# Optimization experiments

Hardware: AMD Instinct MI355X
Metric: run time of the kernel (lower is better)

The kernel has to match this reference:

```python
import jax, jax.numpy as jnp
import numpy as np


def setup_inputs() -> dict:
    key = jax.random.key(0)
    k1, k2 = jax.random.split(key)
    B, S, F = 8, 2048, 128
    feature = jax.random.normal(k1, (B, S, F), dtype=jnp.float32)
    noise = jax.random.normal(k2, (B, S, S), dtype=jnp.float32)
    return {"feature": feature, "noise": noise}


def reference(feature, noise):
    # stability: inverse variance over feat dim (torch.var is unbiased -> ddof=1)
    var = jnp.var(feature, axis=2, ddof=1, keepdims=True)          # [B, S, 1]
    stability = 1.0 / (var + 1e-6)
    stability = stability / jnp.max(stability)                      # global max normalize
    # scale per-row noise and softmax over keys (last dim)
    scaled = noise * stability                                      # [B, S, S]
    path = jax.nn.softmax(scaled, axis=-1)                          # [B, S, S]
    # weighted sum of frames
    return jnp.einsum('bij,bjf->bif', path, feature)                # [B, S, F]
```

## Files before the change

### kernel.cpp

```cpp
#include <hip/hip_runtime.h>
#include <hip/hip_bf16.h>

#define BATCH 8
#define SEQ   2048
#define FEATD 128
#define IBLK  32
#define JT    64
#define EPAD  72
#define FPAD  72

typedef __attribute__((ext_vector_type(8))) short short8;
typedef __attribute__((ext_vector_type(4))) float f32x4;

__device__ __forceinline__ unsigned short f2bf(float f) {
  unsigned int u = __float_as_uint(f);
  u += 0x7fffu + ((u >> 16) & 1u);
  return (unsigned short)(u >> 16);
}

__global__ __launch_bounds__(256)
void prep_kernel(const float* __restrict__ feature,
                 float* __restrict__ stab,
                 unsigned int* __restrict__ gmax,
                 unsigned short* __restrict__ featT) {
  __shared__ float tile[32][132];
  __shared__ float wmax[4];
  int bid = blockIdx.x;
  int b   = bid >> 6;
  int j0  = (bid & 63) * 32;
  int t   = threadIdx.x;
  int r   = t >> 3;
  int seg = t & 7;

  const float* rp = feature + ((size_t)(b * SEQ + j0 + r)) * FEATD + seg * 16;
  float s = 0.0f, ss = 0.0f;
  #pragma unroll
  for (int k = 0; k < 4; k++) {
    float4 v = ((const float4*)rp)[k];
    tile[r][seg * 16 + k * 4 + 0] = v.x;
    tile[r][seg * 16 + k * 4 + 1] = v.y;
    tile[r][seg * 16 + k * 4 + 2] = v.z;
    tile[r][seg * 16 + k * 4 + 3] = v.w;
    s  += v.x + v.y + v.z + v.w;
    ss += v.x * v.x + v.y * v.y + v.z * v.z + v.w * v.w;
  }
  #pragma unroll
  for (int d = 1; d < 8; d <<= 1) {
    s  += __shfl_xor(s, d, 8);
    ss += __shfl_xor(ss, d, 8);
  }
  float st = 0.0f;
  if (seg == 0) {
    float var = (ss - s * s * (1.0f / 128.0f)) * (1.0f / 127.0f);
    st = 1.0f / (var + 1e-6f);
    stab[(size_t)b * SEQ + j0 + r] = st;
  }
  float m = st;
  #pragma unroll
  for (int d = 1; d < 64; d <<= 1) m = fmaxf(m, __shfl_xor(m, d, 64));
  if ((t & 63) == 0) wmax[t >> 6] = m;
  __syncthreads();
  if (t == 0) {
    float mm = fmaxf(fmaxf(wmax[0], wmax[1]), fmaxf(wmax[2], wmax[3]));
    atomicMax(gmax, __float_as_uint(mm));
  }
  int f  = t >> 1;
  int jh = t & 1;
  unsigned short obuf[16];
  #pragma unroll
  for (int jj = 0; jj < 16; jj++) obuf[jj] = f2bf(tile[jh * 16 + jj][f]);
  unsigned short* dst = featT + ((size_t)(b * FEATD + f)) * SEQ + j0 + jh * 16;
  *(uint4*)(dst)     = *(const uint4*)&obuf[0];
  *(uint4*)(dst + 8) = *(const uint4*)&obuf[8];
}

#define LOADN(JTV, N0, N1) { const float4* p_ = (const float4*)(nrow + (size_t)(JTV) * JT); N0 = p_[0]; N1 = p_[1]; }
#define LOADF(JTV, F0, F1, F2, F3) { const uint4* p_ = (const uint4*)(frow + (size_t)(JTV) * JT); F0 = p_[0]; F1 = p_[1]; F2 = p_[2]; F3 = p_[3]; }
#define PROC(N0, N1, SLOT) { \
    float x_[8] = {N0.x, N0.y, N0.z, N0.w, N1.x, N1.y, N1.z, N1.w}; \
    short8 eh_; \
    _Pragma("unroll") \
    for (int k_ = 0; k_ < 8; k_++) { \
      float e_ = __expf(x_[k_] * sn); \
      unsigned short h_ = f2bf(e_); \
      eh_[k_] = (short)h_; \
      psum += __uint_as_float(((unsigned int)h_) << 16); \
    } \
    *(short8*)&e_lds[SLOT][ei][ejg * 8] = eh_; }
#define STOREF(SLOT, F0, F1, F2, F3) { \
    uint4* fd_ = (uint4*)&fT[SLOT][ff][fh * 32]; \
    fd_[0] = F0; fd_[1] = F1; fd_[2] = F2; fd_[3] = F3; }
#define DOMFMA(SLOT) { \
    _Pragma("unroll") \
    for (int ks = 0; ks < 2; ks++) { \
      short8 a_ = *(const short8*)&e_lds[SLOT][wi + l15][ks * 32 + lg * 8]; \
      _Pragma("unroll") \
      for (int fc = 0; fc < 4; fc++) { \
        short8 b_ = *(const short8*)&fT[SLOT][wf + fc * 16 + l15][ks * 32 + lg * 8]; \
        acc[fc] = __builtin_amdgcn_mfma_f32_16x16x32_bf16(a_, b_, acc[fc], 0, 0, 0); \
      } \
    } }

__global__ __launch_bounds__(256, 2)
void fused_kernel(const float* __restrict__ noise,
                  const unsigned short* __restrict__ featT,
                  const float* __restrict__ stab,
                  const unsigned int* __restrict__ gmaxp,
                  float* __restrict__ out) {
  __shared__ unsigned short e_lds[2][IBLK][EPAD];
  __shared__ unsigned short fT[2][FEATD][FPAD];
  __shared__ float snorm[IBLK];
  __shared__ float rowsum[IBLK];

  int bid = blockIdx.x;
  int b   = bid >> 6;
  int i0  = (bid & 63) * IBLK;
  int t   = threadIdx.x;

  float gmaxv = __uint_as_float(*gmaxp);
  if (t < IBLK) snorm[t] = stab[(size_t)b * SEQ + i0 + t] / gmaxv;
  __syncthreads();

  int ei  = t >> 3;
  int ejg = t & 7;
  const float* nrow = noise + ((size_t)b * SEQ + i0 + ei) * SEQ + ejg * 8;
  float sn = snorm[ei];

  int ff = t >> 1;
  int fh = t & 1;
  const unsigned short* frow = featT + ((size_t)b * FEATD + ff) * SEQ + fh * 32;

  int wv   = t >> 6;
  int lane = t & 63;
  int wi   = (wv >> 1) * 16;
  int wf   = (wv & 1) * 64;
  int l15  = lane & 15;
  int lg   = lane >> 4;

  f32x4 acc[4];
  #pragma unroll
  for (int k = 0; k < 4; k++) {
    f32x4 z = {0.0f, 0.0f, 0.0f, 0.0f};
    acc[k] = z;
  }
  float psum = 0.0f;

  float4 nA0, nA1, nB0, nB1;
  uint4  fA0, fA1, fA2, fA3, fB0, fB1, fB2, fB3;

  LOADN(0, nA0, nA1);
  LOADF(0, fA0, fA1, fA2, fA3);

  for (int jt = 0; jt < SEQ / JT; jt += 2) {
    LOADN(jt + 1, nB0, nB1);
    LOADF(jt + 1, fB0, fB1, fB2, fB3);
    PROC(nA0, nA1, 0);
    STOREF(0, fA0, fA1, fA2, fA3);
    __syncthreads();
    DOMFMA(0);
    if (jt + 2 < SEQ / JT) {
      LOADN(jt + 2, nA0, nA1);
      LOADF(jt + 2, fA0, fA1, fA2, fA3);
    }
    PROC(nB0, nB1, 1);
    STOREF(1, fB0, fB1, fB2, fB3);
    __syncthreads();
    DOMFMA(1);
  }

  psum += __shfl_xor(psum, 1, 64);
  psum += __shfl_xor(psum, 2, 64);
  psum += __shfl_xor(psum, 4, 64);
  if (ejg == 0) rowsum[ei] = psum;
  __syncthreads();

  float* orow = out + ((size_t)b * SEQ + i0 + wi) * FEATD + wf;
  #pragma unroll
  for (int v = 0; v < 4; v++) {
    int r = lg * 4 + v;
    float rinv = 1.0f / rowsum[wi + r];
    #pragma unroll
    for (int fc = 0; fc < 4; fc++) {
      orow[(size_t)r * FEATD + fc * 16 + l15] = acc[fc][v] * rinv;
    }
  }
}

extern "C" void kernel_launch(void* const* d_in, const int* in_sizes, int n_in,
                              void* d_out, int out_size, void* d_ws, size_t ws_size,
                              hipStream_t stream) {
  const float* feature = (const float*)d_in[0];
  const float* noise   = (const float*)d_in[1];
  float* out = (float*)d_out;

  float* stab           = (float*)d_ws;
  unsigned int* gmax    = (unsigned int*)((char*)d_ws + (64 << 10));
  unsigned short* featT = (unsigned short*)((char*)d_ws + (128 << 10));

  hipMemsetAsync(gmax, 0, sizeof(unsigned int), stream);
  prep_kernel<<<dim3(BATCH * SEQ / 32), dim3(256), 0, stream>>>(feature, stab, gmax, featT);
  fused_kernel<<<dim3(BATCH * SEQ / IBLK), dim3(256), 0, stream>>>(noise, featT, stab, gmax, out);
}
```

Before: 218.2 us.

## Fuse prep and softmax-matmul into one cooperative kernel with register-fed MFMA

Merges the stability/transposition prep and the main softmax-weighted matmul into one cooperative kernel separated by a grid-wide sync. It removes the second kernel launch and the global-max dependency gap. The main loop no longer stages exp values and feature tiles through LDS. Each lane builds its MFMA A-fragment from noise directly in registers and reads B-fragments of the transposed bf16 features straight from global memory, which removes the per-tile __syncthreads. In exchange, the two waves sharing a row block each recompute the same exponentials and reread the same noise. Feature fragments now come from L2 as strided loads instead of shared tiles, and the grid must stay fully co-resident for the cooperative launch.

```diff
diff --git a/kernel.cpp b/kernel.cpp
--- a/kernel.cpp
+++ b/kernel.cpp
@@ -1,13 +1,14 @@
 #include <hip/hip_runtime.h>
 #include <hip/hip_bf16.h>
+#include <hip/hip_cooperative_groups.h>
+
+namespace cg = cooperative_groups;
 
 #define BATCH 8
 #define SEQ   2048
 #define FEATD 128
 #define IBLK  32
 #define JT    64
-#define EPAD  72
-#define FPAD  72
 
 typedef __attribute__((ext_vector_type(8))) short short8;
 typedef __attribute__((ext_vector_type(4))) float f32x4;
@@ -18,170 +19,152 @@
   return (unsigned short)(u >> 16);
 }
 
-__global__ __launch_bounds__(256)
-void prep_kernel(const float* __restrict__ feature,
-                 float* __restrict__ stab,
-                 unsigned int* __restrict__ gmax,
-                 unsigned short* __restrict__ featT) {
-  __shared__ float tile[32][132];
-  __shared__ float wmax[4];
-  int bid = blockIdx.x;
-  int b   = bid >> 6;
-  int j0  = (bid & 63) * 32;
-  int t   = threadIdx.x;
-  int r   = t >> 3;
-  int seg = t & 7;
+#define LOADN4(JTV, N0, N1, N2, N3) { \
+    const float4* p_ = (const float4*)(nbase + (size_t)(JTV) * JT); \
+    N0 = p_[0]; N1 = p_[1]; N2 = p_[8]; N3 = p_[9]; }
 
-  const float* rp = feature + ((size_t)(b * SEQ + j0 + r)) * FEATD + seg * 16;
-  float s = 0.0f, ss = 0.0f;
-  #pragma unroll
-  for (int k = 0; k < 4; k++) {
-    float4 v = ((const float4*)rp)[k];
-    tile[r][seg * 16 + k * 4 + 0] = v.x;
-    tile[r][seg * 16 + k * 4 + 1] = v.y;
-    tile[r][seg * 16 + k * 4 + 2] = v.z;
-    tile[r][seg * 16 + k * 4 + 3] = v.w;
-    s  += v.x + v.y + v.z + v.w;
-    ss += v.x * v.x + v.y * v.y + v.z * v.z + v.w * v.w;
-  }
-  #pragma unroll
-  for (int d = 1; d < 8; d <<= 1) {
-    s  += __shfl_xor(s, d, 8);
-    ss += __shfl_xor(ss, d, 8);
-  }
-  float st = 0.0f;
-  if (seg == 0) {
-    float var = (ss - s * s * (1.0f / 128.0f)) * (1.0f / 127.0f);
-    st = 1.0f / (var + 1e-6f);
-    stab[(size_t)b * SEQ + j0 + r] = st;
-  }
-  float m = st;
-  #pragma unroll
-  for (int d = 1; d < 64; d <<= 1) m = fmaxf(m, __shfl_xor(m, d, 64));
-  if ((t & 63) == 0) wmax[t >> 6] = m;
-  __syncthreads();
-  if (t == 0) {
-    float mm = fmaxf(fmaxf(wmax[0], wmax[1]), fmaxf(wmax[2], wmax[3]));
-    atomicMax(gmax, __float_as_uint(mm));
-  }
-  int f  = t >> 1;
-  int jh = t & 1;
-  unsigned short obuf[16];
-  #pragma unroll
-  for (int jj = 0; jj < 16; jj++) obuf[jj] = f2bf(tile[jh * 16 + jj][f]);
-  unsigned short* dst = featT + ((size_t)(b * FEATD + f)) * SEQ + j0 + jh * 16;
-  *(uint4*)(dst)     = *(const uint4*)&obuf[0];
-  *(uint4*)(dst + 8) = *(const uint4*)&obuf[8];
-}
-
-#define LOADN(JTV, N0, N1) { const float4* p_ = (const float4*)(nrow + (size_t)(JTV) * JT); N0 = p_[0]; N1 = p_[1]; }
-#define LOADF(JTV, F0, F1, F2, F3) { const uint4* p_ = (const uint4*)(frow + (size_t)(JTV) * JT); F0 = p_[0]; F1 = p_[1]; F2 = p_[2]; F3 = p_[3]; }
-#define PROC(N0, N1, SLOT) { \
-    float x_[8] = {N0.x, N0.y, N0.z, N0.w, N1.x, N1.y, N1.z, N1.w}; \
-    short8 eh_; \
+#define PROCB(N0, N1, N2, N3, PK0, PK1) { \
+    float x_[16] = {N0.x, N0.y, N0.z, N0.w, N1.x, N1.y, N1.z, N1.w, \
+                    N2.x, N2.y, N2.z, N2.w, N3.x, N3.y, N3.z, N3.w}; \
     _Pragma("unroll") \
     for (int k_ = 0; k_ < 8; k_++) { \
       float e_ = __expf(x_[k_] * sn); \
       unsigned short h_ = f2bf(e_); \
-      eh_[k_] = (short)h_; \
+      PK0[k_] = (short)h_; \
       psum += __uint_as_float(((unsigned int)h_) << 16); \
     } \
-    *(short8*)&e_lds[SLOT][ei][ejg * 8] = eh_; }
-#define STOREF(SLOT, F0, F1, F2, F3) { \
-    uint4* fd_ = (uint4*)&fT[SLOT][ff][fh * 32]; \
-    fd_[0] = F0; fd_[1] = F1; fd_[2] = F2; fd_[3] = F3; }
-#define DOMFMA(SLOT) { \
     _Pragma("unroll") \
-    for (int ks = 0; ks < 2; ks++) { \
-      short8 a_ = *(const short8*)&e_lds[SLOT][wi + l15][ks * 32 + lg * 8]; \
-      _Pragma("unroll") \
-      for (int fc = 0; fc < 4; fc++) { \
-        short8 b_ = *(const short8*)&fT[SLOT][wf + fc * 16 + l15][ks * 32 + lg * 8]; \
-        acc[fc] = __builtin_amdgcn_mfma_f32_16x16x32_bf16(a_, b_, acc[fc], 0, 0, 0); \
-      } \
+    for (int k_ = 0; k_ < 8; k_++) { \
+      float e_ = __expf(x_[8 + k_] * sn); \
+      unsigned short h_ = f2bf(e_); \
+      PK1[k_] = (short)h_; \
+      psum += __uint_as_float(((unsigned int)h_) << 16); \
+    } }
+
+#define MFMAB(PK0, PK1, JTV) { \
+    const unsigned short* fb_ = fbT + (size_t)(JTV) * JT; \
+    _Pragma("unroll") \
+    for (int fc = 0; fc < 4; fc++) { \
+      short8 b0_ = *(const short8*)(fb_ + (size_t)fc * 16 * SEQ); \
+      short8 b1_ = *(const short8*)(fb_ + (size_t)fc * 16 * SEQ + 32); \
+      acc[fc] = __builtin_amdgcn_mfma_f32_16x16x32_bf16(PK0, b0_, acc[fc], 0, 0, 0); \
+      acc[fc] = __builtin_amdgcn_mfma_f32_16x16x32_bf16(PK1, b1_, acc[fc], 0, 0, 0); \
     } }
 
 __global__ __launch_bounds__(256, 2)
-void fused_kernel(const float* __restrict__ noise,
-                  const unsigned short* __restrict__ featT,
-                  const float* __restrict__ stab,
-                  const unsigned int* __restrict__ gmaxp,
-                  float* __restrict__ out) {
-  __shared__ unsigned short e_lds[2][IBLK][EPAD];
-  __shared__ unsigned short fT[2][FEATD][FPAD];
-  __shared__ float snorm[IBLK];
-  __shared__ float rowsum[IBLK];
+void frame_kernel(const float* __restrict__ feature,
+                  const float* __restrict__ noise,
+                  float* __restrict__ out,
+                  float* __restrict__ stab,
+                  unsigned int* __restrict__ gmax,
+                  unsigned short* __restrict__ featT) {
+  __shared__ float tile[32][132];
+  __shared__ float wmax[4];
 
   int bid = blockIdx.x;
-  int b   = bid >> 6;
-  int i0  = (bid & 63) * IBLK;
   int t   = threadIdx.x;
 
-  float gmaxv = __uint_as_float(*gmaxp);
-  if (t < IBLK) snorm[t] = stab[(size_t)b * SEQ + i0 + t] / gmaxv;
-  __syncthreads();
+  {
+    int b  = bid >> 6;
+    int j0 = (bid & 63) * 32;
+    int r  = t >> 3;
+    int seg = t & 7;
 
-  int ei  = t >> 3;
-  int ejg = t & 7;
-  const float* nrow = noise + ((size_t)b * SEQ + i0 + ei) * SEQ + ejg * 8;
-  float sn = snorm[ei];
-
-  int ff = t >> 1;
-  int fh = t & 1;
-  const unsigned short* frow = featT + ((size_t)b * FEATD + ff) * SEQ + fh * 32;
-
-  int wv   = t >> 6;
-  int lane = t & 63;
-  int wi   = (wv >> 1) * 16;
-  int wf   = (wv & 1) * 64;
-  int l15  = lane & 15;
-  int lg   = lane >> 4;
-
-  f32x4 acc[4];
-  #pragma unroll
-  for (int k = 0; k < 4; k++) {
-    f32x4 z = {0.0f, 0.0f, 0.0f, 0.0f};
-    acc[k] = z;
-  }
-  float psum = 0.0f;
-
-  float4 nA0, nA1, nB0, nB1;
-  uint4  fA0, fA1, fA2, fA3, fB0, fB1, fB2, fB3;
-
-  LOADN(0, nA0, nA1);
-  LOADF(0, fA0, fA1, fA2, fA3);
-
-  for (int jt = 0; jt < SEQ / JT; jt += 2) {
-    LOADN(jt + 1, nB0, nB1);
-    LOADF(jt + 1, fB0, fB1, fB2, fB3);
-    PROC(nA0, nA1, 0);
-    STOREF(0, fA0, fA1, fA2, fA3);
+    const float* rp = feature + ((size_t)(b * SEQ + j0 + r)) * FEATD + seg * 16;
+    float s = 0.0f, ss = 0.0f;
+    #pragma unroll
+    for (int k = 0; k < 4; k++) {
+      float4 v = ((const float4*)rp)[k];
+      tile[r][seg * 16 + k * 4 + 0] = v.x;
+      tile[r][seg * 16 + k * 4 + 1] = v.y;
+      tile[r][seg * 16 + k * 4 + 2] = v.z;
+      tile[r][seg * 16 + k * 4 + 3] = v.w;
+      s  += v.x + v.y + v.z + v.w;
+      ss += v.x * v.x + v.y * v.y + v.z * v.z + v.w * v.w;
+    }
+    #pragma unroll
+    for (int d = 1; d < 8; d <<= 1) {
+      s  += __shfl_xor(s, d, 8);
+      ss += __shfl_xor(ss, d, 8);
+    }
+    float st = 0.0f;
+    if (seg == 0) {
+      float var = (ss - s * s * (1.0f / 128.0f)) * (1.0f / 127.0f);
+      st = 1.0f / (var + 1e-6f);
+      stab[(size_t)b * SEQ + j0 + r] = st;
+    }
+    float m = st;
+    #pragma unroll
+    for (int d = 1; d < 64; d <<= 1) m = fmaxf(m, __shfl_xor(m, d, 64));
+    if ((t & 63) == 0) wmax[t >> 6] = m;
     __syncthreads();
-    DOMFMA(0);
-    if (jt + 2 < SEQ / JT) {
-      LOADN(jt + 2, nA0, nA1);
-      LOADF(jt + 2, fA0, fA1, fA2, fA3);
+    if (t == 0) {
+      float mm = fmaxf(fmaxf(wmax[0], wmax[1]), fmaxf(wmax[2], wmax[3]));
+      atomicMax(gmax, __float_as_uint(mm));
     }
-    PROC(nB0, nB1, 1);
-    STOREF(1, fB0, fB1, fB2, fB3);
-    __syncthreads();
-    DOMFMA(1);
+    int f  = t >> 1;
+    int jh = t & 1;
+    unsigned short obuf[16];
+    #pragma unroll
+    for (int jj = 0; jj < 16; jj++) obuf[jj] = f2bf(tile[jh * 16 + jj][f]);
+    unsigned short* dst = featT + ((size_t)(b * FEATD + f)) * SEQ + j0 + jh * 16;
+    *(uint4*)(dst)     = *(const uint4*)&obuf[0];
+    *(uint4*)(dst + 8) = *(const uint4*)&obuf[8];
   }
 
-  psum += __shfl_xor(psum, 1, 64);
-  psum += __shfl_xor(psum, 2, 64);
-  psum += __shfl_xor(psum, 4, 64);
-  if (ejg == 0) rowsum[ei] = psum;
-  __syncthreads();
+  cg::this_grid().sync();
 
-  float* orow = out + ((size_t)b * SEQ + i0 + wi) * FEATD + wf;
-  #pragma unroll
-  for (int v = 0; v < 4; v++) {
-    int r = lg * 4 + v;
-    float rinv = 1.0f / rowsum[wi + r];
+  {
+    int b   = bid >> 6;
+    int i0  = (bid & 63) * IBLK;
+    int wv   = t >> 6;
+    int lane = t & 63;
+    int l15  = lane & 15;
+    int lg   = lane >> 4;
+    int wi   = (wv >> 1) * 16;
+    int wf   = (wv & 1) * 64;
+    int row  = i0 + wi + l15;
+
+    float gmaxv = __uint_as_float(*gmax);
+    float sn = stab[(size_t)b * SEQ + row] / gmaxv;
+
+    const float* nbase = noise + ((size_t)b * SEQ + row) * SEQ + lg * 8;
+    const unsigned short* fbT = featT + (size_t)b * FEATD * SEQ + (size_t)(wf + l15) * SEQ + lg * 8;
+
+    f32x4 acc[4];
     #pragma unroll
-    for (int fc = 0; fc < 4; fc++) {
-      orow[(size_t)r * FEATD + fc * 16 + l15] = acc[fc][v] * rinv;
+    for (int k = 0; k < 4; k++) {
+      f32x4 z = {0.0f, 0.0f, 0.0f, 0.0f};
+      acc[k] = z;
+    }
+    float psum = 0.0f;
+
+    float4 nA0, nA1, nA2, nA3, nB0, nB1, nB2, nB3;
+    short8 pkA0, pkA1, pkB0, pkB1;
+
+    LOADN4(0, nA0, nA1, nA2, nA3);
+    for (int jt = 0; jt < SEQ / JT; jt += 2) {
+      LOADN4(jt + 1, nB0, nB1, nB2, nB3);
+      PROCB(nA0, nA1, nA2, nA3, pkA0, pkA1);
+      MFMAB(pkA0, pkA1, jt);
+      if (jt + 2 < SEQ / JT) { LOADN4(jt + 2, nA0, nA1, nA2, nA3); }
+      PROCB(nB0, nB1, nB2, nB3, pkB0, pkB1);
+      MFMAB(pkB0, pkB1, jt + 1);
+    }
+
+    psum += __shfl_xor(psum, 16, 64);
+    psum += __shfl_xor(psum, 32, 64);
+
+    float* orow = out + ((size_t)b * SEQ + i0 + wi) * FEATD + wf;
+    #pragma unroll
+    for (int v = 0; v < 4; v++) {
+      int r = lg * 4 + v;
+      float rs = __shfl(psum, r, 64);
+      float rinv = 1.0f / rs;
+      #pragma unroll
+      for (int fc = 0; fc < 4; fc++) {
+        orow[(size_t)r * FEATD + fc * 16 + l15] = acc[fc][v] * rinv;
+      }
     }
   }
 }
@@ -198,6 +181,9 @@
   unsigned short* featT = (unsigned short*)((char*)d_ws + (128 << 10));
 
   hipMemsetAsync(gmax, 0, sizeof(unsigned int), stream);
-  prep_kernel<<<dim3(BATCH * SEQ / 32), dim3(256), 0, stream>>>(feature, stab, gmax, featT);
-  fused_kernel<<<dim3(BATCH * SEQ / IBLK), dim3(256), 0, stream>>>(noise, featT, stab, gmax, out);
+
+  void* args[] = { (void*)&feature, (void*)&noise, (void*)&out,
+                   (void*)&stab, (void*)&gmax, (void*)&featT };
+  hipLaunchCooperativeKernel((void*)frame_kernel, dim3(BATCH * SEQ / IBLK), dim3(256),
+                             args, 0, stream);
 }
```

Result: slower. 307.0 us (+40.7%).
